# Performance work log

Hardware: AMD Instinct MI355X
Metric: run time of the kernel (lower is better)

## Reference

```python
import jax, jax.numpy as jnp
import numpy as np

NTOK, NINP, NREL = 50257, 512, 200
N, L, EPS = 1024, 64, 32  # n sequences, seq length, edges per sequence
E = N * EPS               # m.sum()


def setup_inputs() -> dict:
    key = jax.random.key(0)
    k1, k2, k3, k4 = jax.random.split(key, 4)
    seq = jax.random.randint(k1, (N, L), 0, NTOK, dtype=jnp.int32)
    m = jnp.full((N,), EPS, dtype=jnp.int32)          # edges per sequence (constant -> static E)
    rel = jax.random.randint(k2, (E,), 0, NREL, dtype=jnp.int32)
    emb = jax.random.normal(k3, (NTOK, NINP), dtype=jnp.float32)          # nn.Embedding weight
    W = 0.01 * jax.random.normal(k4, (NREL, NINP), dtype=jnp.float32)     # nn.Linear weight
    b = jnp.zeros((NREL,), dtype=jnp.float32)                             # nn.Linear bias
    return {"seq": seq, "m": m, "rel": rel, "emb": emb, "W": W, "b": b}


def reference(seq, m, rel, emb, W, b):
    # logit = linear(embedding(seq).sum(1))
    h = emb[seq].sum(axis=1)                    # (N, NINP) gather + segment-sum over tokens
    logit = h @ W.T + b                         # (N, NREL)

    # multi-label mask: mask[i, r] = True iff some edge of sequence i has relation r
    n_seq = m.shape[0]
    idx = jnp.repeat(jnp.arange(n_seq), m, total_repeat_length=rel.shape[0])  # (E,)
    mask = jnp.zeros((n_seq, logit.shape[1]), dtype=bool).at[idx, rel].set(True)

    # sum of logsigmoid on positive labels + log(1+1e-5 - sigmoid) on negatives, / len(seq)
    logp = jnp.sum(jnp.where(mask,
                             jax.nn.log_sigmoid(logit),
                             jnp.log(1.0 + 1e-5 - jax.nn.sigmoid(logit)))) / seq.shape[0]
    acc = jnp.mean(((logit > 0.5) == mask).astype(jnp.float32))
    return logp, acc
```

## Files before the change

### kernel.cpp

```cpp
#include <hip/hip_runtime.h>

#define NINP 512
#define NREL 200
#define LSEQ 64
#define WT_LD 256
#define SPB 4

__global__ __launch_bounds__(256) void gather_kernel(
    const int* __restrict__ seq,
    const float* __restrict__ emb,
    float4* __restrict__ part,
    int N, int L)
{
    __shared__ int    toks[32];
    __shared__ float4 hpart[2][NINP / 4];

    const int b  = blockIdx.x;
    const int s  = b >> 1;
    const int hs = b & 1;
    const int t  = threadIdx.x;
    const int grp = t >> 7;
    const int e   = t & 127;

    if (t < 32) toks[t] = seq[s * LSEQ + hs * 32 + t];
    __syncthreads();

    float4 acc = make_float4(0.f, 0.f, 0.f, 0.f);
    #pragma unroll
    for (int batch = 0; batch < 2; ++batch) {
        const int base = grp * 16 + batch * 8;
        float4 v[8];
        #pragma unroll
        for (int j = 0; j < 8; ++j) {
            const int tok = __builtin_amdgcn_readfirstlane(toks[base + j]);
            v[j] = ((const float4*)(emb + (long)tok * NINP))[e];
        }
        float4 s01, s23, s45, s67;
        s01.x = v[0].x + v[1].x; s01.y = v[0].y + v[1].y; s01.z = v[0].z + v[1].z; s01.w = v[0].w + v[1].w;
        s23.x = v[2].x + v[3].x; s23.y = v[2].y + v[3].y; s23.z = v[2].z + v[3].z; s23.w = v[2].w + v[3].w;
        s45.x = v[4].x + v[5].x; s45.y = v[4].y + v[5].y; s45.z = v[4].z + v[5].z; s45.w = v[4].w + v[5].w;
        s67.x = v[6].x + v[7].x; s67.y = v[6].y + v[7].y; s67.z = v[6].z + v[7].z; s67.w = v[6].w + v[7].w;
        acc.x += (s01.x + s23.x) + (s45.x + s67.x);
        acc.y += (s01.y + s23.y) + (s45.y + s67.y);
        acc.z += (s01.z + s23.z) + (s45.z + s67.z);
        acc.w += (s01.w + s23.w) + (s45.w + s67.w);
    }
    hpart[grp][e] = acc;
    __syncthreads();

    if (t < 128) {
        float4 lo = hpart[0][t];
        float4 hi = hpart[1][t];
        lo.x += hi.x; lo.y += hi.y; lo.z += hi.z; lo.w += hi.w;
        part[(long)b * 128 + t] = lo;
    }
}

__global__ __launch_bounds__(256) void prep_kernel(
    const float* __restrict__ W,
    const float4* __restrict__ part,
    float* __restrict__ Wt,
    float4* __restrict__ hg4,
    int N)
{
    const int b = blockIdx.x;
    const int t = threadIdx.x;
    if (b < NINP / 2) {
        #pragma unroll
        for (int j = 0; j < 2; ++j) {
            const int k = b * 2 + j;
            Wt[k * WT_LD + t] = (t < NREL) ? W[t * NINP + k] : 0.f;
        }
    } else {
        const int bb = b - NINP / 2;
        #pragma unroll
        for (int j = 0; j < 2; ++j) {
            const long idx = (long)bb * 512 + j * 256 + t;
            const long s = idx >> 7;
            const long e = idx & 127;
            float4 lo = part[s * 256 + e];
            float4 hi = part[s * 256 + 128 + e];
            lo.x += hi.x; lo.y += hi.y; lo.z += hi.z; lo.w += hi.w;
            hg4[idx] = lo;
        }
    }
}

__global__ __launch_bounds__(256) void loss_kernel(
    const float* __restrict__ hg,
    const float* __restrict__ Wt,
    const int* __restrict__ rel,
    const float* __restrict__ bias,
    float* __restrict__ out,
    int N, int eps)
{
    __shared__ unsigned int maskbits[SPB][8];
    __shared__ float red_logp[4];
    __shared__ float red_acc[4];

    const int i0 = blockIdx.x * SPB;
    const int t  = threadIdx.x;

    if (t < SPB * 8) maskbits[t >> 3][t & 7] = 0u;
    __syncthreads();
    if (t < SPB * 32) {
        const int s = t >> 5, j = t & 31;
        if (j < eps) {
            int r = rel[(i0 + s) * eps + j];
            atomicOr(&maskbits[s][r >> 5], 1u << (r & 31));
        }
    }
    __syncthreads();

    const float* __restrict__ h0p = hg + (long)(i0 + 0) * NINP;
    const float* __restrict__ h1p = hg + (long)(i0 + 1) * NINP;
    const float* __restrict__ h2p = hg + (long)(i0 + 2) * NINP;
    const float* __restrict__ h3p = hg + (long)(i0 + 3) * NINP;

    float d0 = 0.f, d1 = 0.f, d2 = 0.f, d3 = 0.f;
    #pragma unroll 8
    for (int k = 0; k < NINP; ++k) {
        const float wt = Wt[k * WT_LD + t];
        d0 += wt * h0p[k];
        d1 += wt * h1p[k];
        d2 += wt * h2p[k];
        d3 += wt * h3p[k];
    }

    float term = 0.f, match = 0.f;
    if (t < NREL) {
        const float bt = bias[t];
        float dots[SPB] = {d0 + bt, d1 + bt, d2 + bt, d3 + bt};
        #pragma unroll
        for (int s = 0; s < SPB; ++s) {
            const float dot = dots[s];
            const unsigned mb = (maskbits[s][t >> 5] >> (t & 31)) & 1u;
            float tr;
            if (mb) {
                tr = fminf(dot, 0.f) - log1pf(expf(-fabsf(dot)));
            } else {
                tr = logf(1e-5f + 1.f / (1.f + expf(dot)));
            }
            term  += tr;
            match += (((dot > 0.5f) ? 1u : 0u) == mb) ? 1.f : 0.f;
        }
    }

    #pragma unroll
    for (int off = 32; off > 0; off >>= 1) {
        term  += __shfl_down(term,  off);
        match += __shfl_down(match, off);
    }
    const int wave = t >> 6;
    const int lane = t & 63;
    if (lane == 0) { red_logp[wave] = term; red_acc[wave] = match; }
    __syncthreads();
    if (t == 0) {
        float s = red_logp[0] + red_logp[1] + red_logp[2] + red_logp[3];
        float a = red_acc[0]  + red_acc[1]  + red_acc[2]  + red_acc[3];
        atomicAdd(out + 0, s / (float)N);
        atomicAdd(out + 1, a / ((float)N * (float)NREL));
    }
}

extern "C" void kernel_launch(void* const* d_in, const int* in_sizes, int n_in,
                              void* d_out, int out_size, void* d_ws, size_t ws_size,
                              hipStream_t stream) {
    const int*   seq = (const int*)d_in[0];
    const int*   m   = (const int*)d_in[1]; (void)m;
    const int*   rel = (const int*)d_in[2];
    const float* emb = (const float*)d_in[3];
    const float* W   = (const float*)d_in[4];
    const float* b   = (const float*)d_in[5];
    float* out = (float*)d_out;

    const int N   = in_sizes[1];
    const int L   = in_sizes[0] / N;
    const int eps = in_sizes[2] / N;

    float4* part = (float4*)d_ws;
    float*  hg   = (float*)((char*)d_ws + (size_t)4 * 1024 * 1024);
    float*  Wt   = (float*)((char*)d_ws + (size_t)6 * 1024 * 1024);

    hipMemsetAsync(out, 0, 2 * sizeof(float), stream);
    gather_kernel<<<N * 2, 256, 0, stream>>>(seq, emb, part, N, L);
    prep_kernel<<<NINP / 2 + N / 4, 256, 0, stream>>>(W, part, Wt, (float4*)hg, N);
    loss_kernel<<<N / SPB, 256, 0, stream>>>(hg, Wt, rel, b, out, N, eps);
}
```

Before: 192.3 us.

## Fold prep into gather and loss kernels, split loss dot over k-slices

Moves the W transpose into extra blocks of the gather kernel and the partial-sum combine into the loss kernel, which stages the 4 hidden vectors in LDS. The loss kernel now uses 1024 threads, splitting the 512-long dot product into 4 k-slices that are reduced through shared memory. This removes one kernel launch and the hg round trip through global memory, and raises parallelism in the matvec. In exchange it uses more LDS per block and adds an extra LDS reduction step.

```diff
diff --git a/kernel.cpp b/kernel.cpp
--- a/kernel.cpp
+++ b/kernel.cpp
@@ -6,19 +6,32 @@
 #define WT_LD 256
 #define SPB 4
 
-__global__ __launch_bounds__(256) void gather_kernel(
+__global__ __launch_bounds__(256) void gather_prep_kernel(
     const int* __restrict__ seq,
     const float* __restrict__ emb,
+    const float* __restrict__ W,
     float4* __restrict__ part,
+    float* __restrict__ Wt,
     int N, int L)
 {
+    const int b = blockIdx.x;
+    const int t = threadIdx.x;
+
+    if (b < NINP / 2) {
+        #pragma unroll
+        for (int j = 0; j < 2; ++j) {
+            const int k = b * 2 + j;
+            Wt[k * WT_LD + t] = (t < NREL) ? W[t * NINP + k] : 0.f;
+        }
+        return;
+    }
+
     __shared__ int    toks[32];
     __shared__ float4 hpart[2][NINP / 4];
 
-    const int b  = blockIdx.x;
-    const int s  = b >> 1;
-    const int hs = b & 1;
-    const int t  = threadIdx.x;
+    const int gb = b - NINP / 2;
+    const int s  = gb >> 1;
+    const int hs = gb & 1;
     const int grp = t >> 7;
     const int e   = t & 127;
 
@@ -52,56 +65,36 @@
         float4 lo = hpart[0][t];
         float4 hi = hpart[1][t];
         lo.x += hi.x; lo.y += hi.y; lo.z += hi.z; lo.w += hi.w;
-        part[(long)b * 128 + t] = lo;
+        part[(long)gb * 128 + t] = lo;
     }
 }
 
-__global__ __launch_bounds__(256) void prep_kernel(
-    const float* __restrict__ W,
+__global__ __launch_bounds__(1024) void loss_kernel(
     const float4* __restrict__ part,
-    float* __restrict__ Wt,
-    float4* __restrict__ hg4,
-    int N)
-{
-    const int b = blockIdx.x;
-    const int t = threadIdx.x;
-    if (b < NINP / 2) {
-        #pragma unroll
-        for (int j = 0; j < 2; ++j) {
-            const int k = b * 2 + j;
-            Wt[k * WT_LD + t] = (t < NREL) ? W[t * NINP + k] : 0.f;
-        }
-    } else {
-        const int bb = b - NINP / 2;
-        #pragma unroll
-        for (int j = 0; j < 2; ++j) {
-            const long idx = (long)bb * 512 + j * 256 + t;
-            const long s = idx >> 7;
-            const long e = idx & 127;
-            float4 lo = part[s * 256 + e];
-            float4 hi = part[s * 256 + 128 + e];
-            lo.x += hi.x; lo.y += hi.y; lo.z += hi.z; lo.w += hi.w;
-            hg4[idx] = lo;
-        }
-    }
-}
-
-__global__ __launch_bounds__(256) void loss_kernel(
-    const float* __restrict__ hg,
     const float* __restrict__ Wt,
     const int* __restrict__ rel,
     const float* __restrict__ bias,
     float* __restrict__ out,
     int N, int eps)
 {
+    __shared__ float h_lds[SPB][NINP];
     __shared__ unsigned int maskbits[SPB][8];
-    __shared__ float red_logp[4];
-    __shared__ float red_acc[4];
+    __shared__ float pd[SPB][4][256];
+    __shared__ float red_logp[16];
+    __shared__ float red_acc[16];
 
     const int i0 = blockIdx.x * SPB;
     const int t  = threadIdx.x;
 
-    if (t < SPB * 8) maskbits[t >> 3][t & 7] = 0u;
+    if (t < 512) {
+        const int s = t >> 7, e = t & 127;
+        float4 lo = part[(long)(i0 + s) * 256 + e];
+        float4 hi = part[(long)(i0 + s) * 256 + 128 + e];
+        float4 c;
+        c.x = lo.x + hi.x; c.y = lo.y + hi.y; c.z = lo.z + hi.z; c.w = lo.w + hi.w;
+        ((float4*)h_lds)[t] = c;
+    }
+    if (t >= 512 && t < 512 + SPB * 8) ((unsigned int*)maskbits)[t - 512] = 0u;
     __syncthreads();
     if (t < SPB * 32) {
         const int s = t >> 5, j = t & 31;
@@ -110,30 +103,43 @@
             atomicOr(&maskbits[s][r >> 5], 1u << (r & 31));
         }
     }
+
+    const int kslice = t >> 8;
+    const int r      = t & 255;
+    float d0 = 0.f, d1 = 0.f, d2 = 0.f, d3 = 0.f;
+    const float4* h40 = (const float4*)h_lds[0];
+    const float4* h41 = (const float4*)h_lds[1];
+    const float4* h42 = (const float4*)h_lds[2];
+    const float4* h43 = (const float4*)h_lds[3];
+    #pragma unroll 4
+    for (int k4 = kslice * 32; k4 < kslice * 32 + 32; ++k4) {
+        const int k = k4 * 4;
+        const float w0 = Wt[(k + 0) * WT_LD + r];
+        const float w1 = Wt[(k + 1) * WT_LD + r];
+        const float w2 = Wt[(k + 2) * WT_LD + r];
+        const float w3 = Wt[(k + 3) * WT_LD + r];
+        const float4 hv0 = h40[k4];
+        const float4 hv1 = h41[k4];
+        const float4 hv2 = h42[k4];
+        const float4 hv3 = h43[k4];
+        d0 += w0 * hv0.x + w1 * hv0.y + w2 * hv0.z + w3 * hv0.w;
+        d1 += w0 * hv1.x + w1 * hv1.y + w2 * hv1.z + w3 * hv1.w;
+        d2 += w0 * hv2.x + w1 * hv2.y + w2 * hv2.z + w3 * hv2.w;
+        d3 += w0 * hv3.x + w1 * hv3.y + w2 * hv3.z + w3 * hv3.w;
+    }
+    pd[0][kslice][r] = d0;
+    pd[1][kslice][r] = d1;
+    pd[2][kslice][r] = d2;
+    pd[3][kslice][r] = d3;
     __syncthreads();
-
-    const float* __restrict__ h0p = hg + (long)(i0 + 0) * NINP;
-    const float* __restrict__ h1p = hg + (long)(i0 + 1) * NINP;
-    const float* __restrict__ h2p = hg + (long)(i0 + 2) * NINP;
-    const float* __restrict__ h3p = hg + (long)(i0 + 3) * NINP;
-
-    float d0 = 0.f, d1 = 0.f, d2 = 0.f, d3 = 0.f;
-    #pragma unroll 8
-    for (int k = 0; k < NINP; ++k) {
-        const float wt = Wt[k * WT_LD + t];
-        d0 += wt * h0p[k];
-        d1 += wt * h1p[k];
-        d2 += wt * h2p[k];
-        d3 += wt * h3p[k];
-    }
 
     float term = 0.f, match = 0.f;
     if (t < NREL) {
         const float bt = bias[t];
-        float dots[SPB] = {d0 + bt, d1 + bt, d2 + bt, d3 + bt};
         #pragma unroll
         for (int s = 0; s < SPB; ++s) {
-            const float dot = dots[s];
+            const float dot = ((pd[s][0][t] + pd[s][1][t]) +
+                               (pd[s][2][t] + pd[s][3][t])) + bt;
             const unsigned mb = (maskbits[s][t >> 5] >> (t & 31)) & 1u;
             float tr;
             if (mb) {
@@ -156,8 +162,9 @@
     if (lane == 0) { red_logp[wave] = term; red_acc[wave] = match; }
     __syncthreads();
     if (t == 0) {
-        float s = red_logp[0] + red_logp[1] + red_logp[2] + red_logp[3];
-        float a = red_acc[0]  + red_acc[1]  + red_acc[2]  + red_acc[3];
+        float s = 0.f, a = 0.f;
+        #pragma unroll
+        for (int w = 0; w < 16; ++w) { s += red_logp[w]; a += red_acc[w]; }
         atomicAdd(out + 0, s / (float)N);
         atomicAdd(out + 1, a / ((float)N * (float)NREL));
     }
@@ -179,11 +186,9 @@
     const int eps = in_sizes[2] / N;
 
     float4* part = (float4*)d_ws;
-    float*  hg   = (float*)((char*)d_ws + (size_t)4 * 1024 * 1024);
-    float*  Wt   = (float*)((char*)d_ws + (size_t)6 * 1024 * 1024);
+    float*  Wt   = (float*)((char*)d_ws + (size_t)4 * 1024 * 1024);
 
     hipMemsetAsync(out, 0, 2 * sizeof(float), stream);
-    gather_kernel<<<N * 2, 256, 0, stream>>>(seq, emb, part, N, L);
-    prep_kernel<<<NINP / 2 + N / 4, 256, 0, stream>>>(W, part, Wt, (float4*)hg, N);
-    loss_kernel<<<N / SPB, 256, 0, stream>>>(hg, Wt, rel, b, out, N, eps);
+    gather_prep_kernel<<<NINP / 2 + N * 2, 256, 0, stream>>>(seq, emb, W, part, Wt, N, L);
+    loss_kernel<<<N / SPB, 1024, 0, stream>>>(part, Wt, rel, b, out, N, eps);
 }
```

Result: faster. 181.9 us (-5.4%).
